# Performance work log

Measured on AMD Instinct MI355X. Metric: run time of the kernel, lower is better.

## Reference

```python
import jax, jax.numpy as jnp
import numpy as np

NR, NU, NS, NO = 4096, 4, 8, 8
RHO_SR, RHO_A, SIGMA, ALPHA, SIGMA_B = 0.8, 0.02, 0.084, 0.6, 1.6
BATCH, SEQ = 16, 1024


def _make_reservoir_matrix(rng):
    # Sparse random recurrent matrix: density RHO_A, rescaled to spectral radius RHO_SR.
    A = rng.uniform(-1.0, 1.0, size=(NR, NR)) * (rng.random((NR, NR)) < RHO_A)
    # Power iteration to estimate spectral radius (largest |eigenvalue|).
    v = rng.standard_normal(NR)
    for _ in range(100):
        v = A @ v
        v = v / (np.linalg.norm(v) + 1e-30)
    sr = np.linalg.norm(A @ v)
    return (A * (RHO_SR / (sr + 1e-30))).astype(np.float32)


def setup_inputs() -> dict:
    key = jax.random.key(0)
    k1, = jax.random.split(key, 1)
    rng = np.random.default_rng(0)
    inp = jax.random.normal(k1, (BATCH, SEQ, NU + NS), dtype=jnp.float32)
    r_0 = jnp.zeros((1, BATCH, NR), dtype=jnp.float32)
    A = jnp.asarray(_make_reservoir_matrix(rng))                                  # (Nr, Nr)
    B = jnp.asarray(SIGMA * rng.uniform(-1.0, 1.0, size=(NR, NU + NS)), jnp.float32)  # input matrix
    b = jnp.asarray(SIGMA_B * rng.uniform(-1.0, 1.0, size=(NR,)), jnp.float32)    # additive bias
    C_w = jnp.asarray(rng.standard_normal((NO, NR)) / np.sqrt(NR), jnp.float32)   # readout (no bias)
    return {"input": inp, "r_0": r_0, "A": A, "B": B, "b": b, "C_w": C_w}


def reference(input, r_0, A, B, b, C_w):
    # Leaky-integrator ESN recurrence over the sequence, then linear readout on the
    # final reservoir state:  r_{t+1} = (1-alpha) r_t + alpha * tanh(A r_t + B x_t + b)
    # Precompute input projections for all steps: (B, S, Nr) -> scan axis first.
    proj = jnp.einsum("bsf,nf->sbn", input, B) + b  # (S, batch, Nr)

    def step(r, p_t):
        r_new = (1.0 - ALPHA) * r + ALPHA * jnp.tanh(r @ A.T + p_t)
        return r_new, None

    r_n, _ = jax.lax.scan(step, r_0[0], proj)  # (batch, Nr)
    return r_n @ C_w.T  # (batch, No)
```

## Files before the change

kernel.cpp:

```cpp
#include <hip/hip_runtime.h>
#include <hip/hip_bf16.h>
#include <stdint.h>

#define NRR     4096
#define NBATCH  16
#define NFEAT   12
#define SEQLEN  1024
#define ALPHA_C 0.6f

typedef _Float16 f16x8 __attribute__((ext_vector_type(8)));
typedef _Float16 f16x2 __attribute__((ext_vector_type(2)));
typedef float    f32x4 __attribute__((ext_vector_type(4)));
typedef unsigned long long u64;

constexpr int WGS    = 256;
constexpr int TPB    = 512;
constexpr int WAVES  = 8;
constexpr int KCHUNK = NRR / WAVES;
constexpr int FRAGS  = KCHUNK / 32;
constexpr int NFLAG  = 16;
constexpr int SLOTE  = NBATCH * NRR;

#define SC_AGENT __HIP_MEMORY_SCOPE_AGENT

__device__ __forceinline__ unsigned ld_rlx(const unsigned* p) {
    return __hip_atomic_load(p, __ATOMIC_RELAXED, SC_AGENT);
}
__device__ __forceinline__ u64 ld_rlx64(const void* p) {
    return __hip_atomic_load((const u64*)p, __ATOMIC_RELAXED, SC_AGENT);
}
__device__ __forceinline__ void st_rlx(unsigned* p, unsigned v) {
    __hip_atomic_store(p, v, __ATOMIC_RELAXED, SC_AGENT);
}
__device__ __forceinline__ void st_rlx_f32(float* p, float v) {
    __hip_atomic_store(p, v, __ATOMIC_RELAXED, SC_AGENT);
}

__device__ __forceinline__ void gridbar(unsigned* slots, unsigned* flags,
                                        unsigned epoch, int wg, int tid,
                                        int lane, int wave, int use_inv) {
    __syncthreads();
    if (tid == 0) {
        if (use_inv)
            (void)__hip_atomic_load(&slots[wg], __ATOMIC_ACQUIRE, SC_AGENT);
        st_rlx(&slots[wg], epoch);
    }
    if ((wg | wave) == 0) {
        const u64* sp = (const u64*)slots;
        const int i0 = lane * 2;
        for (;;) {
            u64 a = ld_rlx64(&sp[i0]);
            u64 b = ld_rlx64(&sp[i0 + 1]);
            bool ok = ((unsigned)a >= epoch) & ((unsigned)(a >> 32) >= epoch) &
                      ((unsigned)b >= epoch) & ((unsigned)(b >> 32) >= epoch);
            if (__all(ok)) break;
            __builtin_amdgcn_s_sleep(1);
        }
        if (lane < NFLAG) st_rlx(&flags[lane * 32], epoch);
    } else {
        const unsigned* f = &flags[(wg & (NFLAG - 1)) * 32];
        while (ld_rlx(f) < epoch) __builtin_amdgcn_s_sleep(1);
    }
    asm volatile("" ::: "memory");
}

__global__ __launch_bounds__(TPB, 1) void esn_persistent(
    const float* __restrict__ x,
    const float* __restrict__ r0,
    const float* __restrict__ A,
    const float* __restrict__ Bm,
    const float* __restrict__ bias,
    const float* __restrict__ Cw,
    float* __restrict__ out,
    unsigned* __restrict__ slots,
    unsigned* __restrict__ flags,
    _Float16* __restrict__ rbuf,
    float* __restrict__ rfin,
    int use_inv)
{
    const int wg    = blockIdx.x;
    const int tid   = threadIdx.x;
    const int wave  = tid >> 6;
    const int lane  = tid & 63;
    const int l15   = lane & 15;
    const int g     = lane >> 4;
    const int nbase = wg * 16;

    __shared__ float lds_red[WAVES][16][16];
    __shared__ float lds_x[2][NBATCH][NFEAT];
    __shared__ float lds_Bp[16][NFEAT];
    __shared__ float lds_bias[16];
    __shared__ float lds_out[4][128];

    uint4 afrag[FRAGS];
    {
        const float* arow = A + (size_t)(nbase + l15) * NRR + wave * KCHUNK + g * 8;
#pragma unroll
        for (int i = 0; i < FRAGS; ++i) {
            const float4* p = (const float4*)(arow + i * 32);
            float4 f0 = p[0];
            float4 f1 = p[1];
            f16x8 h;
            h[0] = (_Float16)f0.x; h[1] = (_Float16)f0.y;
            h[2] = (_Float16)f0.z; h[3] = (_Float16)f0.w;
            h[4] = (_Float16)f1.x; h[5] = (_Float16)f1.y;
            h[6] = (_Float16)f1.z; h[7] = (_Float16)f1.w;
            afrag[i] = __builtin_bit_cast(uint4, h);
        }
    }

    const int xb = tid / NFEAT;
    const int xf = tid % NFEAT;
    const size_t xofs = (size_t)xb * SEQLEN * NFEAT + xf;

    if (tid < 16 * NFEAT)
        lds_Bp[xb][xf] = Bm[(size_t)(nbase + xb) * NFEAT + xf];
    if (tid < 16)
        lds_bias[tid] = bias[nbase + tid];
    if (tid < NBATCH * NFEAT)
        lds_x[0][xb][xf] = x[xofs];

    const int ub = tid >> 4;
    const int un = tid & 15;
    float rm = 0.0f;
    if (tid < 256) {
        rm = r0[ub * NRR + nbase + un];
        float hi = __shfl_down(rm, 1);
        if (!(un & 1)) {
            f16x2 h2; h2[0] = (_Float16)rm; h2[1] = (_Float16)hi;
            st_rlx((unsigned*)(rbuf + (size_t)ub * NRR + nbase + un),
                   __builtin_bit_cast(unsigned, h2));
        }
    }

    gridbar(slots, flags, 1u, wg, tid, lane, wave, use_inv);

    const size_t roff = (size_t)l15 * NRR + wave * KCHUNK + g * 8;

    for (int t = 0; t < SEQLEN; ++t) {
        const _Float16* rcur = rbuf + (size_t)(use_inv ? (t & 1) : t) * SLOTE;
        _Float16*       rnxt = rbuf + (size_t)(use_inv ? ((t + 1) & 1) : (t + 1)) * SLOTE;

        float xp = 0.0f;
        if (tid < NBATCH * NFEAT && t + 1 < SEQLEN)
            xp = x[xofs + (size_t)(t + 1) * NFEAT];

        f32x4 acc = {0.f, 0.f, 0.f, 0.f};
        const _Float16* rrow = rcur + roff;
#pragma unroll
        for (int i = 0; i < FRAGS; ++i) {
            uint4 u = *(const uint4*)(rrow + i * 32);
            acc = __builtin_amdgcn_mfma_f32_16x16x32_f16(
                __builtin_bit_cast(f16x8, afrag[i]),
                __builtin_bit_cast(f16x8, u), acc, 0, 0, 0);
        }
        *(f32x4*)&lds_red[wave][l15][g * 4] = acc;
        __syncthreads();

        if (tid < 256) {
            float s = 0.f;
#pragma unroll
            for (int w = 0; w < WAVES; ++w) s += lds_red[w][ub][un];
            float p = lds_bias[un];
            const float* xr = lds_x[t & 1][ub];
#pragma unroll
            for (int f = 0; f < NFEAT; ++f) p += lds_Bp[un][f] * xr[f];
            rm = (1.0f - ALPHA_C) * rm + ALPHA_C * tanhf(s + p);
            float hi = __shfl_down(rm, 1);
            if (!(un & 1)) {
                f16x2 h2; h2[0] = (_Float16)rm; h2[1] = (_Float16)hi;
                st_rlx((unsigned*)(rnxt + (size_t)ub * NRR + nbase + un),
                       __builtin_bit_cast(unsigned, h2));
            }
            if (t == SEQLEN - 1)
                st_rlx_f32(&rfin[(size_t)ub * NRR + nbase + un], rm);
        }
        if (tid < NBATCH * NFEAT && t + 1 < SEQLEN)
            lds_x[(t + 1) & 1][xb][xf] = xp;

        gridbar(slots, flags, (unsigned)(t + 2), wg, tid, lane, wave, use_inv);
    }

    if (wg == 0) {
        const int oi   = tid & 127;
        const int part = tid >> 7;
        const int b = oi >> 3, o = oi & 7;
        const float* rv = rfin + (size_t)b * NRR + part * (NRR / 4);
        const float* cv = Cw   + (size_t)o * NRR + part * (NRR / 4);
        float s = 0.f;
        for (int k = 0; k < NRR / 4; k += 2) {
            u64 u = ld_rlx64(rv + k);
            float ra = __builtin_bit_cast(float, (unsigned)u);
            float rb = __builtin_bit_cast(float, (unsigned)(u >> 32));
            s += ra * cv[k] + rb * cv[k + 1];
        }
        lds_out[part][oi] = s;
        __syncthreads();
        if (tid < 128)
            out[tid] = lds_out[0][tid] + lds_out[1][tid] + lds_out[2][tid] + lds_out[3][tid];
    }
}

extern "C" void kernel_launch(void* const* d_in, const int* in_sizes, int n_in,
                              void* d_out, int out_size, void* d_ws, size_t ws_size,
                              hipStream_t stream) {
    const float* x   = (const float*)d_in[0];
    const float* r0  = (const float*)d_in[1];
    const float* A   = (const float*)d_in[2];
    const float* Bm  = (const float*)d_in[3];
    const float* bv  = (const float*)d_in[4];
    const float* Cw  = (const float*)d_in[5];
    float*       out = (float*)d_out;

    char* ws = (char*)d_ws;
    unsigned*  slots = (unsigned*)ws;
    unsigned*  flags = (unsigned*)(ws + 1024);
    float*     rfin  = (float*)(ws + 4096);
    _Float16*  rbuf  = (_Float16*)(ws + 4096 + 262144);

    const size_t need_stream = 4096 + 262144 + (size_t)(SEQLEN + 1) * SLOTE * 2;
    int use_inv = (ws_size >= need_stream) ? 0 : 1;

    hipMemsetAsync(ws, 0, 4096, stream);

    void* args[] = {(void*)&x, (void*)&r0, (void*)&A, (void*)&Bm, (void*)&bv, (void*)&Cw,
                    (void*)&out, (void*)&slots, (void*)&flags, (void*)&rbuf, (void*)&rfin,
                    (void*)&use_inv};
    hipError_t e = hipLaunchCooperativeKernel((const void*)esn_persistent,
                                              dim3(WGS), dim3(TPB), args, 0, stream);
    if (e != hipSuccess) {
        hipLaunchKernelGGL(esn_persistent, dim3(WGS), dim3(TPB), 0, stream,
                           x, r0, A, Bm, bv, Cw, out, slots, flags, rbuf, rfin, use_inv);
    }
}
```

Baseline: 6.157 ms.

## Replace two-level grid barrier with all-poll barrier and use fast tanh

The grid barrier no longer has workgroup 0 gather all slot arrivals and then broadcast release flags. Instead every workgroup's wave 0 polls all 256 slots directly, with the slots padded to 16 bytes and no sleep between polls. This removes one serial broadcast hop per timestep, at the cost of much more polling traffic on the slot array. Separately, tanhf is replaced by a clamped exp/rcp approximation to shorten the per-step elementwise tail.

```diff
diff --git a/kernel.cpp b/kernel.cpp
--- a/kernel.cpp
+++ b/kernel.cpp
@@ -18,7 +18,6 @@
 constexpr int WAVES  = 8;
 constexpr int KCHUNK = NRR / WAVES;
 constexpr int FRAGS  = KCHUNK / 32;
-constexpr int NFLAG  = 16;
 constexpr int SLOTE  = NBATCH * NRR;
 
 #define SC_AGENT __HIP_MEMORY_SCOPE_AGENT
@@ -36,32 +35,32 @@
     __hip_atomic_store(p, v, __ATOMIC_RELAXED, SC_AGENT);
 }
 
-__device__ __forceinline__ void gridbar(unsigned* slots, unsigned* flags,
-                                        unsigned epoch, int wg, int tid,
-                                        int lane, int wave, int use_inv) {
+__device__ __forceinline__ void gridbar(unsigned* slots, unsigned epoch,
+                                        int wg, int tid, int lane, int wave,
+                                        int use_inv) {
     __syncthreads();
-    if (tid == 0) {
-        if (use_inv)
-            (void)__hip_atomic_load(&slots[wg], __ATOMIC_ACQUIRE, SC_AGENT);
-        st_rlx(&slots[wg], epoch);
-    }
-    if ((wg | wave) == 0) {
-        const u64* sp = (const u64*)slots;
-        const int i0 = lane * 2;
+    if (tid == 0) st_rlx(&slots[wg * 4], epoch);
+    if (wave == 0) {
+        const int i0 = lane * 4;
         for (;;) {
-            u64 a = ld_rlx64(&sp[i0]);
-            u64 b = ld_rlx64(&sp[i0 + 1]);
-            bool ok = ((unsigned)a >= epoch) & ((unsigned)(a >> 32) >= epoch) &
-                      ((unsigned)b >= epoch) & ((unsigned)(b >> 32) >= epoch);
+            unsigned a = ld_rlx(&slots[(i0 + 0) * 4]);
+            unsigned b = ld_rlx(&slots[(i0 + 1) * 4]);
+            unsigned c = ld_rlx(&slots[(i0 + 2) * 4]);
+            unsigned d = ld_rlx(&slots[(i0 + 3) * 4]);
+            bool ok = (a >= epoch) & (b >= epoch) & (c >= epoch) & (d >= epoch);
             if (__all(ok)) break;
-            __builtin_amdgcn_s_sleep(1);
-        }
-        if (lane < NFLAG) st_rlx(&flags[lane * 32], epoch);
-    } else {
-        const unsigned* f = &flags[(wg & (NFLAG - 1)) * 32];
-        while (ld_rlx(f) < epoch) __builtin_amdgcn_s_sleep(1);
-    }
+        }
+        if (use_inv && lane == 0)
+            (void)__hip_atomic_load(&slots[wg * 4], __ATOMIC_ACQUIRE, SC_AGENT);
+    }
+    __syncthreads();
     asm volatile("" ::: "memory");
+}
+
+__device__ __forceinline__ float fast_tanh(float v) {
+    float vc = fminf(fmaxf(v, -10.0f), 10.0f);
+    float e  = __expf(2.0f * vc);
+    return (e - 1.0f) * __builtin_amdgcn_rcpf(e + 1.0f);
 }
 
 __global__ __launch_bounds__(TPB, 1) void esn_persistent(
@@ -73,7 +72,6 @@
     const float* __restrict__ Cw,
     float* __restrict__ out,
     unsigned* __restrict__ slots,
-    unsigned* __restrict__ flags,
     _Float16* __restrict__ rbuf,
     float* __restrict__ rfin,
     int use_inv)
@@ -133,7 +131,7 @@
         }
     }
 
-    gridbar(slots, flags, 1u, wg, tid, lane, wave, use_inv);
+    gridbar(slots, 1u, wg, tid, lane, wave, use_inv);
 
     const size_t roff = (size_t)l15 * NRR + wave * KCHUNK + g * 8;
 
@@ -165,7 +163,7 @@
             const float* xr = lds_x[t & 1][ub];
 #pragma unroll
             for (int f = 0; f < NFEAT; ++f) p += lds_Bp[un][f] * xr[f];
-            rm = (1.0f - ALPHA_C) * rm + ALPHA_C * tanhf(s + p);
+            rm = (1.0f - ALPHA_C) * rm + ALPHA_C * fast_tanh(s + p);
             float hi = __shfl_down(rm, 1);
             if (!(un & 1)) {
                 f16x2 h2; h2[0] = (_Float16)rm; h2[1] = (_Float16)hi;
@@ -178,7 +176,7 @@
         if (tid < NBATCH * NFEAT && t + 1 < SEQLEN)
             lds_x[(t + 1) & 1][xb][xf] = xp;
 
-        gridbar(slots, flags, (unsigned)(t + 2), wg, tid, lane, wave, use_inv);
+        gridbar(slots, (unsigned)(t + 2), wg, tid, lane, wave, use_inv);
     }
 
     if (wg == 0) {
@@ -214,7 +212,6 @@
 
     char* ws = (char*)d_ws;
     unsigned*  slots = (unsigned*)ws;
-    unsigned*  flags = (unsigned*)(ws + 1024);
     float*     rfin  = (float*)(ws + 4096);
     _Float16*  rbuf  = (_Float16*)(ws + 4096 + 262144);
 
@@ -224,12 +221,12 @@
     hipMemsetAsync(ws, 0, 4096, stream);
 
     void* args[] = {(void*)&x, (void*)&r0, (void*)&A, (void*)&Bm, (void*)&bv, (void*)&Cw,
-                    (void*)&out, (void*)&slots, (void*)&flags, (void*)&rbuf, (void*)&rfin,
+                    (void*)&out, (void*)&slots, (void*)&rbuf, (void*)&rfin,
                     (void*)&use_inv};
     hipError_t e = hipLaunchCooperativeKernel((const void*)esn_persistent,
                                               dim3(WGS), dim3(TPB), args, 0, stream);
     if (e != hipSuccess) {
         hipLaunchKernelGGL(esn_persistent, dim3(WGS), dim3(TPB), 0, stream,
-                           x, r0, A, Bm, bv, Cw, out, slots, flags, rbuf, rfin, use_inv);
-    }
-}
+                           x, r0, A, Bm, bv, Cw, out, slots, rbuf, rfin, use_inv);
+    }
+}
```

After: 6.244 ms. No clear change (+1.4%).
